# Performance work log

Measured on AMD Instinct MI355X. Metric: run time of the kernel, lower is better.

## Reference

```python
import jax, jax.numpy as jnp
import numpy as np

B, N, H, L, R, E = 8, 10000, 64, 4, 3, 200000
FP, NUM_CELLS = 2048, 100
LN_EPS = 1e-3  # Keras LayerNormalization default epsilon


def setup_inputs() -> dict:
    key = jax.random.key(0)
    ks = jax.random.split(key, 24)
    g = lambda k, shape, fan: (jax.random.uniform(k, shape, jnp.float32) * 2 - 1) * np.sqrt(6.0 / fan)
    inp = {
        'ctl_expr': jax.random.normal(ks[0], (B, N), jnp.float32),
        'drug_targets': jax.random.uniform(ks[1], (B, N), jnp.float32),
        'drug_fp': jax.random.uniform(ks[2], (B, FP), jnp.float32),
        'edge_weight': jax.random.uniform(ks[3], (R, E), jnp.float32),
        'cell_idx': jax.random.randint(ks[4], (B,), 0, NUM_CELLS, jnp.int32),
        'edge_index': jax.random.randint(ks[5], (R, 2, E), 0, N, jnp.int32),
        # parameters
        'W_se': g(ks[6], (1, H), 1 + H),
        'b_se': jnp.zeros((H,), jnp.float32),
        'cell_emb': jax.random.normal(ks[7], (NUM_CELLS, H), jnp.float32) * 0.05,
        'W_f1': g(ks[8], (FP, H), FP + H),
        'b_f1': jnp.zeros((H,), jnp.float32),
        'W_f2': g(ks[9], (H, 2 * H), 3 * H) * 0.1,
        'b_f2': jnp.zeros((2 * H,), jnp.float32),
        'Wself': jnp.stack([g(ks[10 + l], (H, H), 2 * H) for l in range(L)]),
        'Wrel': jnp.stack([jnp.stack([g(jax.random.fold_in(ks[14], l * R + r), (H, H), 2 * H) for r in range(R)]) for l in range(L)]),
        'ln_g': jnp.ones((L, H), jnp.float32),
        'ln_b': jnp.zeros((L, H), jnp.float32),
        'W_out': g(ks[15], (H, 1), H + 1),
        'b_out': jnp.zeros((1,), jnp.float32),
    }
    return inp


def reference(ctl_expr, drug_targets, drug_fp, edge_weight, cell_idx, edge_index,
              W_se, b_se, cell_emb, W_f1, b_f1, W_f2, b_f2,
              Wself, Wrel, ln_g, ln_b, W_out, b_out):
    # shared_embedding: Dense(H, relu) applied to scalar node features
    def shared(v):  # v: [B,N] -> [B,N,H]
        return jax.nn.relu(v[..., None] * W_se[0] + b_se)

    x = shared(ctl_expr) + shared(drug_targets)            # [B,N,H]
    x = x + cell_emb[cell_idx][:, None, :]                 # cell embedding broadcast

    # drug FiLM: gamma/beta conditioning
    film = jax.nn.relu(drug_fp @ W_f1 + b_f1) @ W_f2 + b_f2  # [B,2H]
    gamma, beta = jnp.split(film, 2, axis=-1)
    gamma = jnp.tanh(gamma)
    x = x * (1.0 + gamma[:, None, :]) + beta[:, None, :]

    n_layers, n_rel = Wself.shape[0], Wrel.shape[1]
    for l in range(n_layers):
        out = x @ Wself[l]                                 # self projection [B,N,H]
        for r in range(n_rel):
            src, dst = edge_index[r, 0], edge_index[r, 1]
            h = x @ Wrel[l, r]                             # [B,N,H]
            msg = edge_weight[r][None, :, None] * h[:, src, :]  # [B,E,H]
            out = out.at[:, dst].add(msg)                  # scatter-add to dst nodes
        # LayerNorm over feature dim (Keras eps=1e-3)
        mu = out.mean(-1, keepdims=True)
        var = ((out - mu) ** 2).mean(-1, keepdims=True)
        out = (out - mu) * jax.lax.rsqrt(var + LN_EPS) * ln_g[l] + ln_b[l]
        x = jax.nn.relu(out)

    return (x @ W_out)[..., 0] + b_out[0]                  # [B,N]
```

## Files before the change

### kernel.cpp

```cpp
#include <hip/hip_runtime.h>
#include <hip/hip_bf16.h>
#include <math.h>

#define Bk 8
#define Nk 10000
#define Hk 64
#define Lk 4
#define Rk 3
#define Ek 200000
#define FPk 2048

#define CNTB ((Rk*Ek + 255)/256)
#define INITB 2048

typedef unsigned short u16;
typedef unsigned int   u32;
typedef _Float16 f16;
typedef __attribute__((ext_vector_type(2))) _Float16 f16x2;
typedef __attribute__((ext_vector_type(8))) _Float16 f16x8;
typedef __attribute__((ext_vector_type(4))) float f32x4;

__device__ __forceinline__ f16x2 as_h2(u32 u){
    union{u32 i; f16x2 h;} v; v.i = u; return v.h;
}
__device__ __forceinline__ u32 as_u32(f16x2 h){
    union{u32 i; f16x2 h;} v; v.h = h; return v.i;
}
__device__ __forceinline__ u16 f2h_bits(float f){
    union{f16 h; u16 u;} v; v.h = (f16)f; return v.u;
}

__global__ void k_wprep(const float* __restrict__ Wself, const float* __restrict__ Wrel,
                        u16* __restrict__ wt, int* __restrict__ deg){
    int idx = blockIdx.x*256 + threadIdx.x;
    if(idx < Rk*Nk) deg[idx] = 0;
    if(idx >= Lk*4*2*4*64*8) return;
    int j    = idx & 7;
    int lane = (idx >> 3) & 63;
    int jt   = (idx >> 9) & 3;
    int kc   = (idx >> 11) & 1;
    int mt   = (idx >> 12) & 3;
    int l    = idx >> 14;
    int k    = kc*32 + (lane >> 4)*8 + j;
    int col  = jt*16 + (lane & 15);
    float w = (mt == 0) ? Wself[(l*64 + k)*64 + col]
                        : Wrel[((l*3 + (mt-1))*64 + k)*64 + col];
    wt[idx] = f2h_bits(w);
}

__global__ void k_count_film1(const int* __restrict__ edge_index, int* __restrict__ deg,
                              const float* __restrict__ fp, const float* __restrict__ W1,
                              const float* __restrict__ b1, float* __restrict__ hid){
    __shared__ float red[256];
    if(blockIdx.x < CNTB){
        int idx = blockIdx.x*256 + threadIdx.x;
        if(idx >= Rk*Ek) return;
        int r = idx / Ek, e = idx % Ek;
        int dst = edge_index[r*2*Ek + Ek + e];
        atomicAdd(&deg[r*Nk + dst], 1);
    }else{
        int bb = blockIdx.x - CNTB;
        int b = bb >> 6, h = bb & 63;
        const float* fpb = fp + b*FPk;
        float acc = 0.f;
        for(int k = threadIdx.x; k < FPk; k += 256)
            acc += fpb[k] * W1[k*64 + h];
        red[threadIdx.x] = acc;
        __syncthreads();
        for(int s = 128; s >= 1; s >>= 1){
            if(threadIdx.x < s) red[threadIdx.x] += red[threadIdx.x + s];
            __syncthreads();
        }
        if(threadIdx.x == 0) hid[b*64 + h] = fmaxf(red[0] + b1[h], 0.f);
    }
}

__global__ void k_scan_film2(const int* __restrict__ deg, int* __restrict__ offs,
                             int* __restrict__ cursor,
                             const float* __restrict__ hid, const float* __restrict__ W2,
                             const float* __restrict__ b2,
                             float* __restrict__ g1p, float* __restrict__ beta){
    __shared__ int s[1024];
    if(blockIdx.x < 3){
        int r = blockIdx.x;
        int t = threadIdx.x;
        int base_i = t*10;
        int local[10];
        int sum = 0;
        if(base_i < Nk){
            #pragma unroll
            for(int k = 0; k < 10; ++k){ local[k] = deg[r*Nk + base_i + k]; sum += local[k]; }
        }
        s[t] = sum;
        __syncthreads();
        for(int d = 1; d < 1024; d <<= 1){
            int v = (t >= d) ? s[t-d] : 0;
            __syncthreads();
            s[t] += v;
            __syncthreads();
        }
        if(base_i < Nk){
            int excl = s[t] - sum;
            #pragma unroll
            for(int k = 0; k < 10; ++k){
                offs[r*(Nk+1) + base_i + k] = excl;
                cursor[r*Nk + base_i + k]   = excl;
                excl += local[k];
            }
        }
        if(t == 1023) offs[r*(Nk+1) + Nk] = s[1023];
    }else{
        int b = blockIdx.x - 3;
        int j = threadIdx.x;
        if(j < 128){
            float acc = b2[j];
            for(int k = 0; k < 64; ++k)
                acc += hid[b*64 + k] * W2[k*128 + j];
            if(j < 64) g1p[b*64 + j] = 1.f + tanhf(acc);
            else       beta[b*64 + j - 64] = acc;
        }
    }
}

__global__ void k_fill_init(const int* __restrict__ edge_index, const float* __restrict__ edge_weight,
                            int* __restrict__ cursor, int2* __restrict__ epack,
                            const float* __restrict__ ctl, const float* __restrict__ dt,
                            const int* __restrict__ cell_idx,
                            const float* __restrict__ W_se, const float* __restrict__ b_se,
                            const float* __restrict__ cell_emb,
                            const float* __restrict__ g1p, const float* __restrict__ beta,
                            u16* __restrict__ xh){
    if(blockIdx.x < CNTB){
        int idx = blockIdx.x*256 + threadIdx.x;
        if(idx >= Rk*Ek) return;
        int r = idx / Ek, e = idx % Ek;
        int src = edge_index[r*2*Ek + e];
        int dst = edge_index[r*2*Ek + Ek + e];
        int pos = atomicAdd(&cursor[r*Nk + dst], 1);
        f16 h = (f16)edge_weight[r*Ek + e];
        epack[(size_t)r*Ek + pos] = make_int2(src << 7, (int)as_u32((f16x2){h, h}));
    }else{
        const size_t total = (size_t)Bk*Nk*64;
        size_t start = (size_t)(blockIdx.x - CNTB)*256 + threadIdx.x;
        for(size_t i = start; i < total; i += (size_t)INITB*256){
            int h = (int)(i & 63);
            size_t bn = i >> 6;
            int b = (int)(bn / Nk);
            float w = W_se[h], bs = b_se[h];
            float v = fmaxf(ctl[bn]*w + bs, 0.f) + fmaxf(dt[bn]*w + bs, 0.f)
                    + cell_emb[cell_idx[b]*64 + h];
            xh[i] = f2h_bits(v * g1p[b*64 + h] + beta[b*64 + h]);
        }
    }
}

__global__ __launch_bounds__(256) void k_agg(const u16* __restrict__ xh,
                      const int* __restrict__ offs, const int2* __restrict__ epack,
                      u16* __restrict__ aggh){
    __shared__ int2 stash[4][64];
    int bpair = blockIdx.x & 3;
    int grp   = blockIdx.x >> 2;
    int wq    = threadIdx.x >> 6;
    int wid   = grp*4 + wq;
    int lane  = threadIdx.x & 63;
    int fg    = lane & 31;
    int bl    = lane >> 5;
    int b     = bpair*2 + bl;
    int r = wid / Nk, dst = wid % Nk;
    int o0 = offs[r*(Nk+1) + dst], o1 = offs[r*(Nk+1) + dst + 1];
    const int2* ep = epack + (size_t)r*Ek;
    const char* xb = (const char*)xh + (size_t)b*Nk*128 + fg*4;

    f16x2 A = (f16x2){0,0}, C = (f16x2){0,0};
    int2* st = stash[wq];
    for(int base = o0; base < o1; base += 64){
        int j = base + lane;
        if(j < o1) st[lane] = ep[j];
        int cnt = min(o1 - base, 64);
        int t = 0;
        for(; t + 8 <= cnt; t += 8){
            int4 q01 = *(const int4*)&st[t];
            int4 q23 = *(const int4*)&st[t+2];
            int4 q45 = *(const int4*)&st[t+4];
            int4 q67 = *(const int4*)&st[t+6];
            u32 u0 = *(const u32*)(xb + q01.x);
            u32 u1 = *(const u32*)(xb + q01.z);
            u32 u2 = *(const u32*)(xb + q23.x);
            u32 u3 = *(const u32*)(xb + q23.z);
            u32 u4 = *(const u32*)(xb + q45.x);
            u32 u5 = *(const u32*)(xb + q45.z);
            u32 u6 = *(const u32*)(xb + q67.x);
            u32 u7 = *(const u32*)(xb + q67.z);
            A += as_h2(u0)*as_h2(q01.y); C += as_h2(u1)*as_h2(q01.w);
            A += as_h2(u2)*as_h2(q23.y); C += as_h2(u3)*as_h2(q23.w);
            A += as_h2(u4)*as_h2(q45.y); C += as_h2(u5)*as_h2(q45.w);
            A += as_h2(u6)*as_h2(q67.y); C += as_h2(u7)*as_h2(q67.w);
        }
        for(; t + 2 <= cnt; t += 2){
            int4 q01 = *(const int4*)&st[t];
            u32 u0 = *(const u32*)(xb + q01.x);
            u32 u1 = *(const u32*)(xb + q01.z);
            A += as_h2(u0)*as_h2(q01.y); C += as_h2(u1)*as_h2(q01.w);
        }
        if(t < cnt){
            int2 p = st[t];
            u32 u = *(const u32*)(xb + p.x);
            A += as_h2(u)*as_h2(p.y);
        }
    }
    float a0 = (float)A.x + (float)C.x;
    float a1 = (float)A.y + (float)C.y;
    u32 packed = (u32)f2h_bits(a0) | ((u32)f2h_bits(a1) << 16);
    ((u32*)aggh)[(((size_t)r*Bk + b)*Nk + dst)*32 + fg] = packed;
}

__global__ __launch_bounds__(256) void k_proj_mfma(u16* __restrict__ xh,
        const u16* __restrict__ aggh, const u16* __restrict__ wt,
        const float* __restrict__ ln_g, const float* __restrict__ ln_b, int l,
        int last, const float* __restrict__ W_out, const float* __restrict__ b_out,
        float* __restrict__ out){
    int lane = threadIdx.x & 63;
    int wq   = threadIdx.x >> 6;
    int k8   = blockIdx.x & 7;
    int b    = ((k8 & 3) << 1) | (k8 >> 2);
    int tile = blockIdx.x >> 3;
    int n0   = tile*128 + wq*32;
    int mrow = lane & 15;
    int kq   = lane >> 4;
    int nA = n0 + mrow;       if(nA >= Nk) nA = Nk - 1;
    int nB = n0 + 16 + mrow;  if(nB >= Nk) nB = Nk - 1;

    f32x4 accA[4], accB[4];
    #pragma unroll
    for(int jt = 0; jt < 4; ++jt){
        accA[jt] = (f32x4){0.f,0.f,0.f,0.f};
        accB[jt] = (f32x4){0.f,0.f,0.f,0.f};
    }

    const u16* wl = wt + (size_t)l*16384;

    #pragma unroll
    for(int mt = 0; mt < 4; ++mt){
        const u16* basep = (mt == 0)
            ? xh   + (size_t)b*Nk*64
            : aggh + (((size_t)(mt-1)*Bk + b)*Nk)*64;
        const u16* arowA = basep + (size_t)nA*64;
        const u16* arowB = basep + (size_t)nB*64;
        #pragma unroll
        for(int kc = 0; kc < 2; ++kc){
            f16x8 aA = *(const f16x8*)(arowA + kc*32 + kq*8);
            f16x8 aB = *(const f16x8*)(arowB + kc*32 + kq*8);
            #pragma unroll
            for(int jt = 0; jt < 4; ++jt){
                size_t wi = ((size_t)((mt*2 + kc)*4 + jt)*64 + lane)*8;
                f16x8 bfrag = *(const f16x8*)(wl + wi);
                accA[jt] = __builtin_amdgcn_mfma_f32_16x16x32_f16(aA, bfrag, accA[jt], 0, 0, 0);
                accB[jt] = __builtin_amdgcn_mfma_f32_16x16x32_f16(aB, bfrag, accB[jt], 0, 0, 0);
            }
        }
    }

    float gv[4], bv[4], wo[4];
    #pragma unroll
    for(int jt = 0; jt < 4; ++jt){
        int f = jt*16 + mrow;
        gv[jt] = ln_g[l*64 + f];
        bv[jt] = ln_b[l*64 + f];
        wo[jt] = W_out[f];
    }
    float bo = b_out[0];
    u16* xdst = xh + (size_t)b*Nk*64;

    #pragma unroll
    for(int half = 0; half < 2; ++half){
        f32x4* acc = half ? accB : accA;
        int nbase = n0 + half*16;
        #pragma unroll
        for(int v = 0; v < 4; ++v){
            float s1 = acc[0][v] + acc[1][v] + acc[2][v] + acc[3][v];
            float s2 = acc[0][v]*acc[0][v] + acc[1][v]*acc[1][v]
                     + acc[2][v]*acc[2][v] + acc[3][v]*acc[3][v];
            #pragma unroll
            for(int off = 1; off <= 8; off <<= 1){
                s1 += __shfl_xor(s1, off);
                s2 += __shfl_xor(s2, off);
            }
            float mu  = s1 * 0.015625f;
            float var = s2 * 0.015625f - mu*mu;
            float rstd = rsqrtf(var + 1e-3f);
            int node = nbase + kq*4 + v;
            if(!last){
                if(node < Nk){
                    #pragma unroll
                    for(int jt = 0; jt < 4; ++jt){
                        float o = (acc[jt][v] - mu) * rstd * gv[jt] + bv[jt];
                        xdst[(size_t)node*64 + jt*16 + mrow] = f2h_bits(fmaxf(o, 0.f));
                    }
                }
            }else{
                float s3 = 0.f;
                #pragma unroll
                for(int jt = 0; jt < 4; ++jt){
                    float o = (acc[jt][v] - mu) * rstd * gv[jt] + bv[jt];
                    s3 += fmaxf(o, 0.f) * wo[jt];
                }
                #pragma unroll
                for(int off = 1; off <= 8; off <<= 1)
                    s3 += __shfl_xor(s3, off);
                if(mrow == 0 && node < Nk)
                    out[(size_t)b*Nk + node] = s3 + bo;
            }
        }
    }
}

extern "C" void kernel_launch(void* const* d_in, const int* in_sizes, int n_in,
                              void* d_out, int out_size, void* d_ws, size_t ws_size,
                              hipStream_t stream){
    const float* ctl        = (const float*)d_in[0];
    const float* dt         = (const float*)d_in[1];
    const float* drug_fp    = (const float*)d_in[2];
    const float* edge_w     = (const float*)d_in[3];
    const int*   cell_idx   = (const int*)  d_in[4];
    const int*   edge_index = (const int*)  d_in[5];
    const float* W_se       = (const float*)d_in[6];
    const float* b_se       = (const float*)d_in[7];
    const float* cell_emb   = (const float*)d_in[8];
    const float* W_f1       = (const float*)d_in[9];
    const float* b_f1       = (const float*)d_in[10];
    const float* W_f2       = (const float*)d_in[11];
    const float* b_f2       = (const float*)d_in[12];
    const float* Wself      = (const float*)d_in[13];
    const float* Wrel       = (const float*)d_in[14];
    const float* ln_g       = (const float*)d_in[15];
    const float* ln_b       = (const float*)d_in[16];
    const float* W_out      = (const float*)d_in[17];
    const float* b_out      = (const float*)d_in[18];
    float* out = (float*)d_out;

    char* p = (char*)d_ws;
    auto alloc = [&](size_t bytes)->char*{
        char* r = p; p += (bytes + 255) & ~(size_t)255; return r;
    };
    int*   deg    = (int*)  alloc((size_t)Rk*Nk*4);
    int*   cursor = (int*)  alloc((size_t)Rk*Nk*4);
    int*   offs   = (int*)  alloc((size_t)Rk*(Nk+1)*4);
    int2*  epack  = (int2*) alloc((size_t)Rk*Ek*8);
    float* hid    = (float*)alloc((size_t)Bk*64*4);
    float* g1p    = (float*)alloc((size_t)Bk*64*4);
    float* beta   = (float*)alloc((size_t)Bk*64*4);
    u16*   xh     = (u16*)  alloc((size_t)Bk*Nk*64*2);
    u16*   aggh   = (u16*)  alloc((size_t)3*Bk*Nk*64*2);
    u16*   wt     = (u16*)  alloc((size_t)Lk*16384*2);

    k_wprep<<<(Lk*4*2*4*64*8 + 255)/256, 256, 0, stream>>>(Wself, Wrel, wt, deg);

    k_count_film1<<<CNTB + Bk*64, 256, 0, stream>>>(edge_index, deg, drug_fp, W_f1, b_f1, hid);
    k_scan_film2<<<3 + Bk, 1024, 0, stream>>>(deg, offs, cursor, hid, W_f2, b_f2, g1p, beta);
    k_fill_init<<<CNTB + INITB, 256, 0, stream>>>(edge_index, edge_w, cursor, epack,
                                                  ctl, dt, cell_idx, W_se, b_se, cell_emb,
                                                  g1p, beta, xh);

    const int ntile = (Nk + 127)/128;
    for(int l = 0; l < Lk; ++l){
        k_agg<<<4*7500, 256, 0, stream>>>(xh, offs, epack, aggh);
        k_proj_mfma<<<ntile*8, 256, 0, stream>>>(
            xh, aggh, wt, ln_g, ln_b, l,
            (l == Lk-1) ? 1 : 0, W_out, b_out, out);
    }
}
```

Before: 410.0 us.

## Fuse edge aggregation and MFMA projection into one per-layer kernel

```diff
diff --git a/kernel.cpp b/kernel.cpp
--- a/kernel.cpp
+++ b/kernel.cpp
@@ -154,108 +154,111 @@
     }
 }
 
-__global__ __launch_bounds__(256) void k_agg(const u16* __restrict__ xh,
-                      const int* __restrict__ offs, const int2* __restrict__ epack,
-                      u16* __restrict__ aggh){
-    __shared__ int2 stash[4][64];
-    int bpair = blockIdx.x & 3;
-    int grp   = blockIdx.x >> 2;
-    int wq    = threadIdx.x >> 6;
-    int wid   = grp*4 + wq;
-    int lane  = threadIdx.x & 63;
-    int fg    = lane & 31;
-    int bl    = lane >> 5;
-    int b     = bpair*2 + bl;
-    int r = wid / Nk, dst = wid % Nk;
-    int o0 = offs[r*(Nk+1) + dst], o1 = offs[r*(Nk+1) + dst + 1];
-    const int2* ep = epack + (size_t)r*Ek;
-    const char* xb = (const char*)xh + (size_t)b*Nk*128 + fg*4;
-
-    f16x2 A = (f16x2){0,0}, C = (f16x2){0,0};
-    int2* st = stash[wq];
-    for(int base = o0; base < o1; base += 64){
-        int j = base + lane;
-        if(j < o1) st[lane] = ep[j];
-        int cnt = min(o1 - base, 64);
-        int t = 0;
-        for(; t + 8 <= cnt; t += 8){
-            int4 q01 = *(const int4*)&st[t];
-            int4 q23 = *(const int4*)&st[t+2];
-            int4 q45 = *(const int4*)&st[t+4];
-            int4 q67 = *(const int4*)&st[t+6];
-            u32 u0 = *(const u32*)(xb + q01.x);
-            u32 u1 = *(const u32*)(xb + q01.z);
-            u32 u2 = *(const u32*)(xb + q23.x);
-            u32 u3 = *(const u32*)(xb + q23.z);
-            u32 u4 = *(const u32*)(xb + q45.x);
-            u32 u5 = *(const u32*)(xb + q45.z);
-            u32 u6 = *(const u32*)(xb + q67.x);
-            u32 u7 = *(const u32*)(xb + q67.z);
-            A += as_h2(u0)*as_h2(q01.y); C += as_h2(u1)*as_h2(q01.w);
-            A += as_h2(u2)*as_h2(q23.y); C += as_h2(u3)*as_h2(q23.w);
-            A += as_h2(u4)*as_h2(q45.y); C += as_h2(u5)*as_h2(q45.w);
-            A += as_h2(u6)*as_h2(q67.y); C += as_h2(u7)*as_h2(q67.w);
-        }
-        for(; t + 2 <= cnt; t += 2){
-            int4 q01 = *(const int4*)&st[t];
-            u32 u0 = *(const u32*)(xb + q01.x);
-            u32 u1 = *(const u32*)(xb + q01.z);
-            A += as_h2(u0)*as_h2(q01.y); C += as_h2(u1)*as_h2(q01.w);
-        }
-        if(t < cnt){
-            int2 p = st[t];
-            u32 u = *(const u32*)(xb + p.x);
-            A += as_h2(u)*as_h2(p.y);
-        }
-    }
-    float a0 = (float)A.x + (float)C.x;
-    float a1 = (float)A.y + (float)C.y;
-    u32 packed = (u32)f2h_bits(a0) | ((u32)f2h_bits(a1) << 16);
-    ((u32*)aggh)[(((size_t)r*Bk + b)*Nk + dst)*32 + fg] = packed;
-}
-
-__global__ __launch_bounds__(256) void k_proj_mfma(u16* __restrict__ xh,
-        const u16* __restrict__ aggh, const u16* __restrict__ wt,
+__global__ __launch_bounds__(256) void k_layer(
+        const u16* __restrict__ xin, u16* __restrict__ xout,
+        const int* __restrict__ offs, const int2* __restrict__ epack,
+        const u16* __restrict__ wt,
         const float* __restrict__ ln_g, const float* __restrict__ ln_b, int l,
         int last, const float* __restrict__ W_out, const float* __restrict__ b_out,
         float* __restrict__ out){
+    __shared__ u32  aggl[4][3*16*36];
+    __shared__ int2 stash[4][64];
+
+    int b    = blockIdx.x & 7;
+    int tile = blockIdx.x >> 3;
+    int wq   = threadIdx.x >> 6;
     int lane = threadIdx.x & 63;
-    int wq   = threadIdx.x >> 6;
-    int k8   = blockIdx.x & 7;
-    int b    = ((k8 & 3) << 1) | (k8 >> 2);
-    int tile = blockIdx.x >> 3;
-    int n0   = tile*128 + wq*32;
+    int n0   = tile*64 + wq*16;
+    if(n0 >= Nk) return;
+
+    int fg   = lane & 31;
+    int half = lane >> 5;
+    u32*  ag = aggl[wq];
+    int2* st = stash[wq];
+
+    {
+        const char* xb = (const char*)xin + (size_t)b*Nk*128 + fg*4;
+        for(int p = 0; p < 48; ++p){
+            int r    = p >> 4;
+            int node = n0 + (p & 15);
+            int o0 = offs[r*(Nk+1) + node];
+            int o1 = offs[r*(Nk+1) + node + 1];
+            const int2* ep = epack + (size_t)r*Ek;
+            f16x2 A = (f16x2){0,0}, C = (f16x2){0,0};
+            for(int base = o0; base < o1; base += 64){
+                int j = base + lane;
+                if(j < o1) st[lane] = ep[j];
+                int cnt = min(o1 - base, 64);
+                int t = 0;
+                for(; t + 16 <= cnt; t += 16){
+                    int b0 = t + half*8;
+                    int4 q01 = *(const int4*)&st[b0];
+                    int4 q23 = *(const int4*)&st[b0+2];
+                    int4 q45 = *(const int4*)&st[b0+4];
+                    int4 q67 = *(const int4*)&st[b0+6];
+                    u32 u0 = *(const u32*)(xb + q01.x);
+                    u32 u1 = *(const u32*)(xb + q01.z);
+                    u32 u2 = *(const u32*)(xb + q23.x);
+                    u32 u3 = *(const u32*)(xb + q23.z);
+                    u32 u4 = *(const u32*)(xb + q45.x);
+                    u32 u5 = *(const u32*)(xb + q45.z);
+                    u32 u6 = *(const u32*)(xb + q67.x);
+                    u32 u7 = *(const u32*)(xb + q67.z);
+                    A += as_h2(u0)*as_h2(q01.y); C += as_h2(u1)*as_h2(q01.w);
+                    A += as_h2(u2)*as_h2(q23.y); C += as_h2(u3)*as_h2(q23.w);
+                    A += as_h2(u4)*as_h2(q45.y); C += as_h2(u5)*as_h2(q45.w);
+                    A += as_h2(u6)*as_h2(q67.y); C += as_h2(u7)*as_h2(q67.w);
+                }
+                for(; t + 4 <= cnt; t += 4){
+                    int4 q = *(const int4*)&st[t + half*2];
+                    u32 u0 = *(const u32*)(xb + q.x);
+                    u32 u1 = *(const u32*)(xb + q.z);
+                    A += as_h2(u0)*as_h2(q.y); C += as_h2(u1)*as_h2(q.w);
+                }
+                if(half == 0){
+                    for(; t < cnt; ++t){
+                        int2 q = st[t];
+                        u32 u = *(const u32*)(xb + q.x);
+                        A += as_h2(u)*as_h2(q.y);
+                    }
+                }
+            }
+            float a0 = (float)A.x + (float)C.x;
+            float a1 = (float)A.y + (float)C.y;
+            a0 += __shfl_xor(a0, 32);
+            a1 += __shfl_xor(a1, 32);
+            if(half == 0)
+                ag[p*36 + fg] = (u32)f2h_bits(a0) | ((u32)f2h_bits(a1) << 16);
+        }
+    }
+
     int mrow = lane & 15;
     int kq   = lane >> 4;
-    int nA = n0 + mrow;       if(nA >= Nk) nA = Nk - 1;
-    int nB = n0 + 16 + mrow;  if(nB >= Nk) nB = Nk - 1;
-
-    f32x4 accA[4], accB[4];
-    #pragma unroll
-    for(int jt = 0; jt < 4; ++jt){
-        accA[jt] = (f32x4){0.f,0.f,0.f,0.f};
-        accB[jt] = (f32x4){0.f,0.f,0.f,0.f};
-    }
-
-    const u16* wl = wt + (size_t)l*16384;
-
-    #pragma unroll
-    for(int mt = 0; mt < 4; ++mt){
-        const u16* basep = (mt == 0)
-            ? xh   + (size_t)b*Nk*64
-            : aggh + (((size_t)(mt-1)*Bk + b)*Nk)*64;
-        const u16* arowA = basep + (size_t)nA*64;
-        const u16* arowB = basep + (size_t)nB*64;
+    f32x4 acc[4];
+    #pragma unroll
+    for(int jt = 0; jt < 4; ++jt) acc[jt] = (f32x4){0.f,0.f,0.f,0.f};
+
+    const u16* wl   = wt + (size_t)l*16384;
+    const u16* arow = xin + ((size_t)b*Nk + n0 + mrow)*64;
+
+    #pragma unroll
+    for(int kc = 0; kc < 2; ++kc){
+        f16x8 aA = *(const f16x8*)(arow + kc*32 + kq*8);
+        #pragma unroll
+        for(int jt = 0; jt < 4; ++jt){
+            f16x8 bfrag = *(const f16x8*)(wl + ((size_t)(kc*4 + jt)*64 + lane)*8);
+            acc[jt] = __builtin_amdgcn_mfma_f32_16x16x32_f16(aA, bfrag, acc[jt], 0, 0, 0);
+        }
+    }
+    #pragma unroll
+    for(int mt = 1; mt < 4; ++mt){
         #pragma unroll
         for(int kc = 0; kc < 2; ++kc){
-            f16x8 aA = *(const f16x8*)(arowA + kc*32 + kq*8);
-            f16x8 aB = *(const f16x8*)(arowB + kc*32 + kq*8);
+            f16x8 aA = *(const f16x8*)&ag[((mt-1)*16 + mrow)*36 + kc*16 + kq*4];
             #pragma unroll
             for(int jt = 0; jt < 4; ++jt){
-                size_t wi = ((size_t)((mt*2 + kc)*4 + jt)*64 + lane)*8;
-                f16x8 bfrag = *(const f16x8*)(wl + wi);
-                accA[jt] = __builtin_amdgcn_mfma_f32_16x16x32_f16(aA, bfrag, accA[jt], 0, 0, 0);
-                accB[jt] = __builtin_amdgcn_mfma_f32_16x16x32_f16(aB, bfrag, accB[jt], 0, 0, 0);
+                f16x8 bfrag = *(const f16x8*)(wl + ((size_t)((mt*2 + kc)*4 + jt)*64 + lane)*8);
+                acc[jt] = __builtin_amdgcn_mfma_f32_16x16x32_f16(aA, bfrag, acc[jt], 0, 0, 0);
             }
         }
     }
@@ -269,47 +272,40 @@
         wo[jt] = W_out[f];
     }
     float bo = b_out[0];
-    u16* xdst = xh + (size_t)b*Nk*64;
-
-    #pragma unroll
-    for(int half = 0; half < 2; ++half){
-        f32x4* acc = half ? accB : accA;
-        int nbase = n0 + half*16;
+    u16* xdst = xout + (size_t)b*Nk*64;
+
+    #pragma unroll
+    for(int v = 0; v < 4; ++v){
+        float s1 = acc[0][v] + acc[1][v] + acc[2][v] + acc[3][v];
+        float s2 = acc[0][v]*acc[0][v] + acc[1][v]*acc[1][v]
+                 + acc[2][v]*acc[2][v] + acc[3][v]*acc[3][v];
         #pragma unroll
-        for(int v = 0; v < 4; ++v){
-            float s1 = acc[0][v] + acc[1][v] + acc[2][v] + acc[3][v];
-            float s2 = acc[0][v]*acc[0][v] + acc[1][v]*acc[1][v]
-                     + acc[2][v]*acc[2][v] + acc[3][v]*acc[3][v];
-            #pragma unroll
-            for(int off = 1; off <= 8; off <<= 1){
-                s1 += __shfl_xor(s1, off);
-                s2 += __shfl_xor(s2, off);
-            }
-            float mu  = s1 * 0.015625f;
-            float var = s2 * 0.015625f - mu*mu;
-            float rstd = rsqrtf(var + 1e-3f);
-            int node = nbase + kq*4 + v;
-            if(!last){
-                if(node < Nk){
-                    #pragma unroll
-                    for(int jt = 0; jt < 4; ++jt){
-                        float o = (acc[jt][v] - mu) * rstd * gv[jt] + bv[jt];
-                        xdst[(size_t)node*64 + jt*16 + mrow] = f2h_bits(fmaxf(o, 0.f));
-                    }
-                }
-            }else{
-                float s3 = 0.f;
-                #pragma unroll
-                for(int jt = 0; jt < 4; ++jt){
-                    float o = (acc[jt][v] - mu) * rstd * gv[jt] + bv[jt];
-                    s3 += fmaxf(o, 0.f) * wo[jt];
-                }
-                #pragma unroll
-                for(int off = 1; off <= 8; off <<= 1)
-                    s3 += __shfl_xor(s3, off);
-                if(mrow == 0 && node < Nk)
-                    out[(size_t)b*Nk + node] = s3 + bo;
-            }
+        for(int off = 1; off <= 8; off <<= 1){
+            s1 += __shfl_xor(s1, off);
+            s2 += __shfl_xor(s2, off);
+        }
+        float mu  = s1 * 0.015625f;
+        float var = s2 * 0.015625f - mu*mu;
+        float rstd = rsqrtf(var + 1e-3f);
+        int node = n0 + kq*4 + v;
+        if(!last){
+            #pragma unroll
+            for(int jt = 0; jt < 4; ++jt){
+                float o = (acc[jt][v] - mu) * rstd * gv[jt] + bv[jt];
+                xdst[(size_t)node*64 + jt*16 + mrow] = f2h_bits(fmaxf(o, 0.f));
+            }
+        }else{
+            float s3 = 0.f;
+            #pragma unroll
+            for(int jt = 0; jt < 4; ++jt){
+                float o = (acc[jt][v] - mu) * rstd * gv[jt] + bv[jt];
+                s3 += fmaxf(o, 0.f) * wo[jt];
+            }
+            #pragma unroll
+            for(int off = 1; off <= 8; off <<= 1)
+                s3 += __shfl_xor(s3, off);
+            if(mrow == 0)
+                out[(size_t)b*Nk + node] = s3 + bo;
         }
     }
 }
@@ -349,8 +345,8 @@
     float* hid    = (float*)alloc((size_t)Bk*64*4);
     float* g1p    = (float*)alloc((size_t)Bk*64*4);
     float* beta   = (float*)alloc((size_t)Bk*64*4);
-    u16*   xh     = (u16*)  alloc((size_t)Bk*Nk*64*2);
-    u16*   aggh   = (u16*)  alloc((size_t)3*Bk*Nk*64*2);
+    u16*   xh0    = (u16*)  alloc((size_t)Bk*Nk*64*2);
+    u16*   xh1    = (u16*)  alloc((size_t)Bk*Nk*64*2);
     u16*   wt     = (u16*)  alloc((size_t)Lk*16384*2);
 
     k_wprep<<<(Lk*4*2*4*64*8 + 255)/256, 256, 0, stream>>>(Wself, Wrel, wt, deg);
@@ -359,13 +355,14 @@
     k_scan_film2<<<3 + Bk, 1024, 0, stream>>>(deg, offs, cursor, hid, W_f2, b_f2, g1p, beta);
     k_fill_init<<<CNTB + INITB, 256, 0, stream>>>(edge_index, edge_w, cursor, epack,
                                                   ctl, dt, cell_idx, W_se, b_se, cell_emb,
-                                                  g1p, beta, xh);
-
-    const int ntile = (Nk + 127)/128;
+                                                  g1p, beta, xh0);
+
+    const int ntile = (Nk + 63)/64;
     for(int l = 0; l < Lk; ++l){
-        k_agg<<<4*7500, 256, 0, stream>>>(xh, offs, epack, aggh);
-        k_proj_mfma<<<ntile*8, 256, 0, stream>>>(
-            xh, aggh, wt, ln_g, ln_b, l,
+        u16* xin  = (l & 1) ? xh1 : xh0;
+        u16* xout = (l & 1) ? xh0 : xh1;
+        k_layer<<<ntile*8, 256, 0, stream>>>(
+            xin, xout, offs, epack, wt, ln_g, ln_b, l,
             (l == Lk-1) ? 1 : 0, W_out, b_out, out);
     }
 }
```

Measured after the change: 585.4 us. +42.8%, slower.
